# Kernel tuning notes

Measured on AMD Instinct MI355X. Metric: run time of the kernel, lower is better.

Reference implementation:

```python
import jax, jax.numpy as jnp
import numpy as np

B, C_IN, H, W = 8, 256, 128, 128
N_EXPERTS = 64
TOP_K = 8
ROUTE_SCALE = 1.0
UPDATE_RATE = 0.001
WRAP = 1e8


def setup_inputs() -> dict:
    key = jax.random.key(0)
    k1, k2 = jax.random.split(key)
    x = jax.random.normal(k1, (B, C_IN, H, W), dtype=jnp.float32)
    # conv weight, OIHW, kernel 3x3, no bias (bias=False in module)
    w_gate = jax.random.normal(k2, (N_EXPERTS, C_IN, 3, 3), dtype=jnp.float32) * 0.02
    bias = jnp.zeros((N_EXPERTS,), dtype=jnp.float32)            # routing bias buffer
    history_counts = jnp.zeros((N_EXPERTS,), dtype=jnp.float32)  # load-balance counts buffer
    return {"x": x, "w_gate": w_gate, "bias": bias, "history_counts": history_counts}


def reference(x, w_gate, bias, history_counts):
    # scores = sigmoid(conv3x3(x))  -> (B, E, H, W)
    logits = jax.lax.conv_general_dilated(
        x, w_gate, window_strides=(1, 1), padding=((1, 1), (1, 1)),
        dimension_numbers=("NCHW", "OIHW", "NCHW"))
    scores = jax.nn.sigmoid(logits)

    biased = scores + bias[None, :, None, None]

    # top-k over expert (channel) dim: move experts to last axis
    biased_t = jnp.transpose(biased, (0, 2, 3, 1))   # (B, H, W, E)
    scores_t = jnp.transpose(scores, (0, 2, 3, 1))   # (B, H, W, E)
    _, idx = jax.lax.top_k(biased_t, TOP_K)          # (B, H, W, K) int32

    # gather UNbiased scores at selected experts, softmax over k, scale
    sel = jnp.take_along_axis(scores_t, idx, axis=-1)          # (B, H, W, K)
    weights_t = jax.nn.softmax(sel, axis=-1) * ROUTE_SCALE

    weights = jnp.transpose(weights_t, (0, 3, 1, 2))           # (B, K, H, W)
    indices = jnp.transpose(idx, (0, 3, 1, 2))                 # (B, K, H, W)

    # bincount of selected experts -> history counts update
    counts = history_counts + jnp.bincount(idx.reshape(-1), length=N_EXPERTS).astype(jnp.float32)
    counts = jnp.where(jnp.all(counts > WRAP), jnp.remainder(counts, WRAP), counts)

    # training-mode bias correction: push load toward the mean
    load_diff = counts.mean() - counts
    new_bias = bias + UPDATE_RATE * jnp.sign(load_diff)

    return weights, indices, counts, new_bias
```

## Files before the change

### kernel.cpp

```cpp
#include <hip/hip_runtime.h>

#define BB 8
#define CIN 256
#define NE 64
#define HH 128
#define WW 128
#define HW (HH*WW)
#define TOPK 8

#define TS   16
#define NTH  512
#define HLX  18
#define NSP  (HLX*HLX)
#define NG   (NSP*4)
#define CC   32
#define NCH  (CIN/CC)
#define XROW 32
#define XBUF (NSP*XROW)
#define WCH  (9*NE*XROW)

#define XSWZ(v) (((v) & 15) << 3)

#define W_OFF  0
#define I_OFF  (BB*TOPK*HH*WW)
#define C_OFF  (2*BB*TOPK*HH*WW)
#define NB_OFF (C_OFF + NE)

#define WIMG_BYTES (NCH*WCH)

using f32x4 = __attribute__((ext_vector_type(4))) float;

#define GLDS16(gsrc, ldst) __builtin_amdgcn_global_load_lds( \
    (const __attribute__((address_space(1))) void*)(gsrc),   \
    (__attribute__((address_space(3))) void*)(ldst), 16, 0, 0)

__global__ void prep_w(const float* __restrict__ wg, char* __restrict__ wimg,
                       int* __restrict__ gcount) {
    if (blockIdx.x == 0 && threadIdx.x < NE) gcount[threadIdx.x] = 0;
    int i = blockIdx.x * 256 + threadIdx.x;
    if (i >= NCH * 9 * NE * 8) return;
    int cp = i & 7; int t = i >> 3;
    int e  = t & 63; int t2 = t >> 6;
    int tap = t2 % 9; int c = t2 / 9;
    int ch  = c * CC + cp * 4;
    const float* src = wg + ((size_t)e * CIN + ch) * 9 + tap;
    unsigned u = 0;
    u = __builtin_amdgcn_cvt_pk_fp8_f32(src[0]  * 64.f, src[9]  * 64.f, u, 0);
    u = __builtin_amdgcn_cvt_pk_fp8_f32(src[18] * 64.f, src[27] * 64.f, u, 1);
    int row = tap * 64 + e;
    *(unsigned*)(wimg + (size_t)c * WCH + ((row * 32 + cp * 4) ^ XSWZ(row))) = u;
}

union Smem {
    struct { char xs[2][XBUF]; char wb[2][WCH]; } st;
    float scores[256][65];
};

__global__ __launch_bounds__(NTH, 4) void conv_mfma_kernel(
    const float* __restrict__ x, const char* __restrict__ wimg,
    const float* __restrict__ bias, float* __restrict__ out,
    int* __restrict__ gcount)
{
    __shared__ __align__(16) Smem sm;
    __shared__ int hist[NE];
    __shared__ float sbias[NE];

    const int tid  = threadIdx.x;
    const int lane = tid & 63;
    const int wv   = tid >> 6;
    const int gm   = wv >> 1;
    const int h    = wv & 1;

    const int id  = blockIdx.x;
    const int b   = id & 7;
    const int t   = id >> 3;
    const int by0 = (t >> 3) * TS, bx0 = (t & 7) * TS;
    const float* xb = x + (size_t)b * CIN * HW;

    if (tid < NE) { hist[tid] = 0; sbias[tid] = bias[tid]; }

    const int er = lane & 15;
    const int kg = lane >> 4;

    int srcIdx[3]; int ldsOff[3]; bool okm[3]; bool act[3];
    #pragma unroll
    for (int k = 0; k < 3; ++k) {
        int g  = tid + k * NTH;
        int s  = g % NSP, cp = g / NSP;
        int gy = by0 - 1 + s / HLX, gx = bx0 - 1 + s % HLX;
        act[k] = (g < NG);
        okm[k] = act[k] && ((unsigned)gy < (unsigned)HH) && ((unsigned)gx < (unsigned)WW);
        srcIdx[k] = okm[k] ? (cp * 8 * HW + gy * WW + gx) : 0;
        ldsOff[k] = (s * 32 + cp * 8) ^ XSWZ(s);
    }

    f32x4 acc[4][2];
    #pragma unroll
    for (int m = 0; m < 4; ++m)
        #pragma unroll
        for (int n = 0; n < 2; ++n) acc[m][n] = (f32x4){0.f, 0.f, 0.f, 0.f};

    float xr[3][8];

#define X_ISSUE(cc)                                                         \
    _Pragma("unroll")                                                       \
    for (int k = 0; k < 3; ++k) {                                           \
        if (act[k]) {                                                       \
            const float* p = xb + (size_t)(cc) * (CC * HW) + srcIdx[k];     \
            _Pragma("unroll")                                               \
            for (int q = 0; q < 8; ++q)                                     \
                xr[k][q] = okm[k] ? p[q * HW] : 0.f;                        \
        }                                                                   \
    }

#define X_WRITE(xd)                                                         \
    _Pragma("unroll")                                                       \
    for (int k = 0; k < 3; ++k) {                                           \
        if (act[k]) {                                                       \
            unsigned lo = 0, hi = 0;                                        \
            lo = __builtin_amdgcn_cvt_pk_fp8_f32(xr[k][0], xr[k][1], lo, 0); \
            lo = __builtin_amdgcn_cvt_pk_fp8_f32(xr[k][2], xr[k][3], lo, 1); \
            hi = __builtin_amdgcn_cvt_pk_fp8_f32(xr[k][4], xr[k][5], hi, 0); \
            hi = __builtin_amdgcn_cvt_pk_fp8_f32(xr[k][6], xr[k][7], hi, 1); \
            uint2 u2; u2.x = lo; u2.y = hi;                                 \
            *(uint2*)((xd) + ldsOff[k]) = u2;                               \
        }                                                                   \
    }

#define W_STAGE(cc, wd)                                                     \
    {                                                                       \
        const char* wsrc = wimg + (size_t)(cc) * WCH;                       \
        for (int i = tid; i < WCH / 16; i += NTH)                           \
            GLDS16(wsrc + i * 16, (wd) + i * 16);                           \
    }

#define KX_PHASE(KX, xcur, wcur)                                            \
    {                                                                       \
        long A[6];                                                          \
        _Pragma("unroll")                                                   \
        for (int rr = 0; rr < 6; ++rr) {                                    \
            int s = (gm * 4 + rr) * HLX + er + (KX);                        \
            A[rr] = *(const long*)((xcur) + ((s * 32 + kg * 8) ^ XSWZ(s))); \
        }                                                                   \
        _Pragma("unroll")                                                   \
        for (int ky = 0; ky < 3; ++ky) {                                    \
            const int tap = ky * 3 + (KX);                                  \
            long Bf[2];                                                     \
            _Pragma("unroll")                                               \
            for (int n = 0; n < 2; ++n) {                                   \
                int row = tap * 64 + h * 32 + n * 16 + er;                  \
                Bf[n] = *(const long*)((wcur) + ((row * 32 + kg * 8) ^ XSWZ(row))); \
            }                                                               \
            _Pragma("unroll")                                               \
            for (int n = 0; n < 2; ++n)                                     \
                _Pragma("unroll")                                           \
                for (int m = 0; m < 4; ++m)                                 \
                    acc[m][n] = __builtin_amdgcn_mfma_f32_16x16x32_fp8_fp8(A[m + ky], Bf[n], acc[m][n], 0, 0, 0); \
        }                                                                   \
    }

    X_ISSUE(0)
    W_STAGE(0, sm.st.wb[0])
    X_WRITE(sm.st.xs[0])
    __syncthreads();

    #pragma unroll 1
    for (int c = 0; c < NCH; ++c) {
        char* xcur = sm.st.xs[c & 1];
        char* xalt = sm.st.xs[(c + 1) & 1];
        char* wcur = sm.st.wb[c & 1];
        char* walt = sm.st.wb[(c + 1) & 1];
        const bool more = (c < NCH - 1);

        if (more) {
            X_ISSUE(c + 1)
            W_STAGE(c + 1, walt)
        }
        __builtin_amdgcn_sched_barrier(0);
        KX_PHASE(0, xcur, wcur)
        KX_PHASE(1, xcur, wcur)
        if (more) { X_WRITE(xalt) }
        KX_PHASE(2, xcur, wcur)
        __syncthreads();
    }

    #pragma unroll
    for (int m = 0; m < 4; ++m) {
        int pixbase = (gm * 4 + m) * 16 + kg * 4;
        #pragma unroll
        for (int n = 0; n < 2; ++n) {
            int e = h * 32 + n * 16 + er;
            float bval = sbias[e];
            #pragma unroll
            for (int r = 0; r < 4; ++r)
                sm.scores[pixbase + r][e] =
                    __builtin_amdgcn_rcpf(1.f + __expf(-acc[m][n][r] * 0.015625f)) + bval;
        }
    }
    __syncthreads();

    if (tid < 256) {
        unsigned key[64];
        #pragma unroll
        for (int e = 0; e < 64; ++e)
            key[e] = (__float_as_uint(sm.scores[tid][e]) & ~63u) | (unsigned)(63 - e);

        float selv[TOPK]; int seli[TOPK];
        #pragma unroll
        for (int j = 0; j < TOPK; ++j) {
            unsigned t32[32];
            #pragma unroll
            for (int e = 0; e < 32; ++e) t32[e] = key[2*e] > key[2*e+1] ? key[2*e] : key[2*e+1];
            #pragma unroll
            for (int e = 0; e < 16; ++e) t32[e] = t32[2*e] > t32[2*e+1] ? t32[2*e] : t32[2*e+1];
            #pragma unroll
            for (int e = 0; e < 8; ++e)  t32[e] = t32[2*e] > t32[2*e+1] ? t32[2*e] : t32[2*e+1];
            #pragma unroll
            for (int e = 0; e < 4; ++e)  t32[e] = t32[2*e] > t32[2*e+1] ? t32[2*e] : t32[2*e+1];
            unsigned best = t32[0] > t32[1] ? t32[0] : t32[1];
            unsigned b2   = t32[2] > t32[3] ? t32[2] : t32[3];
            best = best > b2 ? best : b2;

            int e = 63 - (int)(best & 63u);
            seli[j] = e;
            selv[j] = __uint_as_float(best & ~63u) - sbias[e];
            #pragma unroll
            for (int e2 = 0; e2 < 64; ++e2) key[e2] = (key[e2] == best) ? 0u : key[e2];
        }
        float mx = selv[0];
        #pragma unroll
        for (int j = 1; j < TOPK; ++j) mx = fmaxf(mx, selv[j]);
        float ex[TOPK]; float ssum = 0.f;
        #pragma unroll
        for (int j = 0; j < TOPK; ++j) { ex[j] = __expf(selv[j] - mx); ssum += ex[j]; }
        const float inv = 1.f / ssum;

        const int pyg = by0 + (tid >> 4), pxg = bx0 + (tid & 15);
        #pragma unroll
        for (int j = 0; j < TOPK; ++j) {
            size_t o = ((size_t)(b * TOPK + j) * HH + pyg) * WW + pxg;
            out[W_OFF + o] = ex[j] * inv;
            out[I_OFF + o] = (float)seli[j];
            atomicAdd(&hist[seli[j]], 1);
        }
    }
    __syncthreads();
    if (tid < NE) atomicAdd(&gcount[tid], hist[tid]);
}

__global__ void finalize_kernel(const float* __restrict__ bias,
                                const float* __restrict__ history,
                                const int* __restrict__ gcount,
                                float* __restrict__ out)
{
    const int e = threadIdx.x;
    float c = history[e] + (float)gcount[e];
    if (__all(c > 1e8f)) c = fmodf(c, 1e8f);
    float sum = c;
    #pragma unroll
    for (int off = 32; off > 0; off >>= 1) sum += __shfl_down(sum, off);
    float mean = __shfl(sum, 0) * (1.f / 64.f);
    float d = mean - c;
    float sg = (d > 0.f) ? 1.f : ((d < 0.f) ? -1.f : 0.f);
    out[C_OFF + e]  = c;
    out[NB_OFF + e] = bias[e] + 0.001f * sg;
}

extern "C" void kernel_launch(void* const* d_in, const int* in_sizes, int n_in,
                              void* d_out, int out_size, void* d_ws, size_t ws_size,
                              hipStream_t stream) {
    const float* x       = (const float*)d_in[0];
    const float* wg      = (const float*)d_in[1];
    const float* bias    = (const float*)d_in[2];
    const float* history = (const float*)d_in[3];
    float* out = (float*)d_out;

    char* wimg  = (char*)d_ws;
    int* gcount = (int*)((char*)d_ws + WIMG_BYTES);

    prep_w<<<(NCH * 9 * NE * 8 + 255) / 256, 256, 0, stream>>>(wg, wimg, gcount);
    conv_mfma_kernel<<<512, NTH, 0, stream>>>(x, wimg, bias, out, gcount);
    finalize_kernel<<<1, 64, 0, stream>>>(bias, history, gcount, out);
}
```

Measured before the change: 55.15 us.

## Use 16x16x128 scaled FP8 MFMA grouping four taps per instruction

Regroups the 3x3 conv taps so each MFMA covers four taps of 32 channels (K=128) via the scaled f8f6f4 MFMA. Tap 8 stays on the 16x16x32 FP8 MFMA. The weight image and x LDS layout change to match: rows padded to 48/144/40 bytes and the XOR swizzle dropped. This reduces the MFMA instruction count and the number of LDS fragment loads, at the risk of LDS bank conflicts from the padded unswizzled layout and higher register use from 256-bit operands.

Measured after the change: 164.0 us. 2.97x slower.

```diff
diff --git a/kernel.cpp b/kernel.cpp
--- a/kernel.cpp
+++ b/kernel.cpp
@@ -15,11 +15,11 @@
 #define NG   (NSP*4)
 #define CC   32
 #define NCH  (CIN/CC)
-#define XROW 32
+#define XROW 48
 #define XBUF (NSP*XROW)
-#define WCH  (9*NE*XROW)
-
-#define XSWZ(v) (((v) & 15) << 3)
+#define WTG  (64*144)
+#define W8OFF (2*WTG)
+#define WCH  (2*WTG + 64*40)
 
 #define W_OFF  0
 #define I_OFF  (BB*TOPK*HH*WW)
@@ -29,6 +29,11 @@
 #define WIMG_BYTES (NCH*WCH)
 
 using f32x4 = __attribute__((ext_vector_type(4))) float;
+using i32x4 = __attribute__((ext_vector_type(4))) int;
+using i32x8 = __attribute__((ext_vector_type(8))) int;
+
+#define LDB256(PTR) __builtin_shufflevector(*(const i32x4*)(PTR), \
+                    *(const i32x4*)((PTR) + 16), 0, 1, 2, 3, 4, 5, 6, 7)
 
 #define GLDS16(gsrc, ldst) __builtin_amdgcn_global_load_lds( \
     (const __attribute__((address_space(1))) void*)(gsrc),   \
@@ -39,16 +44,18 @@
     if (blockIdx.x == 0 && threadIdx.x < NE) gcount[threadIdx.x] = 0;
     int i = blockIdx.x * 256 + threadIdx.x;
     if (i >= NCH * 9 * NE * 8) return;
-    int cp = i & 7; int t = i >> 3;
+    int cq = i & 7; int t = i >> 3;
     int e  = t & 63; int t2 = t >> 6;
     int tap = t2 % 9; int c = t2 / 9;
-    int ch  = c * CC + cp * 4;
+    int ch  = c * CC + cq * 4;
     const float* src = wg + ((size_t)e * CIN + ch) * 9 + tap;
     unsigned u = 0;
     u = __builtin_amdgcn_cvt_pk_fp8_f32(src[0]  * 64.f, src[9]  * 64.f, u, 0);
     u = __builtin_amdgcn_cvt_pk_fp8_f32(src[18] * 64.f, src[27] * 64.f, u, 1);
-    int row = tap * 64 + e;
-    *(unsigned*)(wimg + (size_t)c * WCH + ((row * 32 + cp * 4) ^ XSWZ(row))) = u;
+    size_t base = (size_t)c * WCH;
+    if (tap < 8) base += (tap >> 2) * WTG + e * 144 + (tap & 3) * 32 + cq * 4;
+    else         base += W8OFF + e * 40 + cq * 4;
+    *(unsigned*)(wimg + base) = u;
 }
 
 union Smem {
@@ -81,6 +88,12 @@
 
     const int er = lane & 15;
     const int kg = lane >> 4;
+
+    const int tap0 = kg,      ky0 = tap0 / 3, kx0 = tap0 - 3 * ky0;
+    const int tap1 = 4 + kg,  ky1 = tap1 / 3, kx1 = tap1 - 3 * ky1;
+    const int abase0 = ky0 * HLX + er + kx0;
+    const int abase1 = ky1 * HLX + er + kx1;
+    const int abase8 = 2 * HLX + er + 2;
 
     int srcIdx[3]; int ldsOff[3]; bool okm[3]; bool act[3];
     #pragma unroll
@@ -91,7 +104,7 @@
         act[k] = (g < NG);
         okm[k] = act[k] && ((unsigned)gy < (unsigned)HH) && ((unsigned)gx < (unsigned)WW);
         srcIdx[k] = okm[k] ? (cp * 8 * HW + gy * WW + gx) : 0;
-        ldsOff[k] = (s * 32 + cp * 8) ^ XSWZ(s);
+        ldsOff[k] = s * XROW + cp * 8;
     }
 
     f32x4 acc[4][2];
@@ -134,28 +147,37 @@
             GLDS16(wsrc + i * 16, (wd) + i * 16);                           \
     }
 
-#define KX_PHASE(KX, xcur, wcur)                                            \
+#define TG_PHASE(ABASE, WOFF, xcur, wcur)                                   \
     {                                                                       \
-        long A[6];                                                          \
+        i32x8 Bf[2];                                                        \
         _Pragma("unroll")                                                   \
-        for (int rr = 0; rr < 6; ++rr) {                                    \
-            int s = (gm * 4 + rr) * HLX + er + (KX);                        \
-            A[rr] = *(const long*)((xcur) + ((s * 32 + kg * 8) ^ XSWZ(s))); \
+        for (int n = 0; n < 2; ++n) {                                       \
+            const char* wp = (wcur) + (WOFF) + (h * 32 + n * 16 + er) * 144 + kg * 32; \
+            Bf[n] = LDB256(wp);                                             \
         }                                                                   \
         _Pragma("unroll")                                                   \
-        for (int ky = 0; ky < 3; ++ky) {                                    \
-            const int tap = ky * 3 + (KX);                                  \
-            long Bf[2];                                                     \
-            _Pragma("unroll")                                               \
-            for (int n = 0; n < 2; ++n) {                                   \
-                int row = tap * 64 + h * 32 + n * 16 + er;                  \
-                Bf[n] = *(const long*)((wcur) + ((row * 32 + kg * 8) ^ XSWZ(row))); \
-            }                                                               \
+        for (int m = 0; m < 4; ++m) {                                       \
+            const char* xp = (xcur) + ((gm * 4 + m) * HLX + (ABASE)) * XROW; \
+            i32x8 Af = LDB256(xp);                                          \
             _Pragma("unroll")                                               \
             for (int n = 0; n < 2; ++n)                                     \
-                _Pragma("unroll")                                           \
-                for (int m = 0; m < 4; ++m)                                 \
-                    acc[m][n] = __builtin_amdgcn_mfma_f32_16x16x32_fp8_fp8(A[m + ky], Bf[n], acc[m][n], 0, 0, 0); \
+                acc[m][n] = __builtin_amdgcn_mfma_scale_f32_16x16x128_f8f6f4( \
+                    Af, Bf[n], acc[m][n], 0, 0, 0, 127, 0, 127);            \
+        }                                                                   \
+    }
+
+#define TAP8_PHASE(xcur, wcur)                                              \
+    {                                                                       \
+        long Bf8[2];                                                        \
+        _Pragma("unroll")                                                   \
+        for (int n = 0; n < 2; ++n)                                         \
+            Bf8[n] = *(const long*)((wcur) + W8OFF + (h * 32 + n * 16 + er) * 40 + kg * 8); \
+        _Pragma("unroll")                                                   \
+        for (int m = 0; m < 4; ++m) {                                       \
+            long Af8 = *(const long*)((xcur) + ((gm * 4 + m) * HLX + abase8) * XROW + kg * 8); \
+            _Pragma("unroll")                                               \
+            for (int n = 0; n < 2; ++n)                                     \
+                acc[m][n] = __builtin_amdgcn_mfma_f32_16x16x32_fp8_fp8(Af8, Bf8[n], acc[m][n], 0, 0, 0); \
         }                                                                   \
     }
 
@@ -177,10 +199,10 @@
             W_STAGE(c + 1, walt)
         }
         __builtin_amdgcn_sched_barrier(0);
-        KX_PHASE(0, xcur, wcur)
-        KX_PHASE(1, xcur, wcur)
+        TG_PHASE(abase0, 0,   xcur, wcur)
+        TG_PHASE(abase1, WTG, xcur, wcur)
         if (more) { X_WRITE(xalt) }
-        KX_PHASE(2, xcur, wcur)
+        TAP8_PHASE(xcur, wcur)
         __syncthreads();
     }
 
```
